# Kernel tuning notes

Hardware: AMD Instinct MI355X
Metric: run time of the kernel (lower is better)

## Reference

```python
import jax, jax.numpy as jnp
import numpy as np

DIM = 2048
DIM_INNER = 4096
D_STATE = 64
D_CONV = 4
HEADDIM = 128
NHEADS = DIM_INNER // HEADDIM  # 32
CHUNK = 256
BATCH = 1
SEQ = 2048
CONV_DIM = DIM_INNER + 2 * D_STATE           # 4224
D_IN_PROJ = 2 * DIM_INNER + 2 * D_STATE + NHEADS  # 8352


def setup_inputs() -> dict:
    key = jax.random.key(0)
    ks = jax.random.split(key, 8)
    x = jax.random.normal(ks[0], (BATCH, SEQ, DIM), jnp.float32)
    in_proj_w = jax.random.normal(ks[1], (D_IN_PROJ, DIM), jnp.float32) * 0.02
    conv_w = jax.random.normal(ks[2], (CONV_DIM, D_CONV), jnp.float32) * 0.2
    conv_b = jnp.zeros((CONV_DIM,), jnp.float32)
    dt_bias = jax.random.normal(ks[3], (NHEADS,), jnp.float32) * 0.1
    A_log = jnp.log(jax.random.uniform(ks[4], (NHEADS,), jnp.float32, 1.0, 16.0))
    D = jnp.ones((NHEADS,), jnp.float32)
    norm_w = jnp.ones((DIM_INNER,), jnp.float32)
    out_proj_w = jax.random.normal(ks[5], (DIM, DIM_INNER), jnp.float32) * 0.02
    return dict(x=x, in_proj_w=in_proj_w, conv_w=conv_w, conv_b=conv_b,
                dt_bias=dt_bias, A_log=A_log, D=D, norm_w=norm_w,
                out_proj_w=out_proj_w)


def _segsum(a):
    # a: [..., T]; out[..., i, j] = sum_{k=j+1..i} a[..., k] for i>=j else -inf
    T = a.shape[-1]
    cs = jnp.cumsum(a, axis=-1)
    seg = cs[..., :, None] - cs[..., None, :]
    mask = jnp.tril(jnp.ones((T, T), bool))
    return jnp.where(mask, seg, -jnp.inf)


def _ssd(x, A, Bm, Cm, chunk):
    # x: [b,l,h,p], A: [b,l,h], Bm/Cm: [b,l,n] (ngroups=1, group dim squeezed)
    b, l, h, p = x.shape
    n = Bm.shape[-1]
    c = l // chunk
    x = x.reshape(b, c, chunk, h, p)
    A = A.reshape(b, c, chunk, h).transpose(0, 3, 1, 2)  # [b,h,c,l]
    Bm = Bm.reshape(b, c, chunk, n)
    Cm = Cm.reshape(b, c, chunk, n)
    A_cumsum = jnp.cumsum(A, axis=-1)                    # [b,h,c,l]
    Lmat = jnp.exp(_segsum(A))                           # [b,h,c,l,l]
    # intra-chunk (diagonal) contribution
    Y_diag = jnp.einsum('bcln,bcsn,bhcls,bcshp->bclhp', Cm, Bm, Lmat, x)
    # per-chunk states
    decay_states = jnp.exp(A_cumsum[..., -1:] - A_cumsum)
    states = jnp.einsum('bcln,bhcl,bclhp->bchpn', Bm, decay_states, x)
    states = jnp.concatenate([jnp.zeros_like(states[:, :1]), states], axis=1)
    # inter-chunk recurrence
    A_last = jnp.pad(A_cumsum[..., -1], ((0, 0), (0, 0), (1, 0)))  # [b,h,c+1]
    decay_chunk = jnp.exp(_segsum(A_last))
    new_states = jnp.einsum('bhzc,bchpn->bzhpn', decay_chunk, states)
    states, final_state = new_states[:, :-1], new_states[:, -1]
    # state -> output (off-diagonal) contribution
    state_decay_out = jnp.exp(A_cumsum)
    Y_off = jnp.einsum('bcln,bchpn,bhcl->bclhp', Cm, states, state_decay_out)
    return (Y_diag + Y_off).reshape(b, l, h, p), final_state


def reference(x, in_proj_w, conv_w, conv_b, dt_bias, A_log, D, norm_w, out_proj_w):
    B, L, _ = x.shape
    zxbcdt = x @ in_proj_w.T                              # [B,L,8352]
    z = zxbcdt[..., :DIM_INNER]
    xBC = zxbcdt[..., DIM_INNER:DIM_INNER + CONV_DIM]
    dt = jax.nn.softplus(zxbcdt[..., -NHEADS:] + dt_bias)  # [B,L,H]
    # causal depthwise conv1d over time (pad d_conv-1 on the left)
    xc = xBC.transpose(0, 2, 1)                           # [B,conv_dim,L]
    xc = jax.lax.conv_general_dilated(
        xc, conv_w[:, None, :], (1,), [(D_CONV - 1, 0)],
        dimension_numbers=('NCH', 'OIH', 'NCH'), feature_group_count=CONV_DIM)
    xc = xc + conv_b[None, :, None]
    xBC = jax.nn.silu(xc).transpose(0, 2, 1)              # [B,L,conv_dim]
    xs = xBC[..., :DIM_INNER].reshape(B, L, NHEADS, HEADDIM)
    Bmat = xBC[..., DIM_INNER:DIM_INNER + D_STATE]
    Cmat = xBC[..., DIM_INNER + D_STATE:]
    A = -jnp.exp(A_log)                                   # [H]
    y, final_state = _ssd(xs * dt[..., None], A * dt, Bmat, Cmat, CHUNK)
    y = y + xs * D[:, None]
    y = y.reshape(B, L, DIM_INNER)
    # gated RMSNorm: x * silu(z), then rms_norm with weight
    g = y * jax.nn.silu(z)
    g = g * jax.lax.rsqrt(jnp.mean(g * g, axis=-1, keepdims=True) + 1e-5) * norm_w
    return g @ out_proj_w.T
```

## Files before the change

kernel.cpp:

```cpp
#include <hip/hip_runtime.h>

typedef short v8s __attribute__((ext_vector_type(8)));
typedef float v4f __attribute__((ext_vector_type(4)));

#define L_SEQ  2048
#define DPROJ  8352
#define CONVD  4224
#define DIN    4096
#define NH     32
#define HD     128
#define NSTATE 64
#define NCHUNK 8
#define CKLEN  256

#define GLOAD_LDS16(gp, lp) \
  __builtin_amdgcn_global_load_lds((const __attribute__((address_space(1))) void*)(gp), \
                                   (__attribute__((address_space(3))) void*)(lp), 16, 0, 0)

__device__ __forceinline__ unsigned short to_bf16(float f) {
  unsigned u = __float_as_uint(f);
  return (unsigned short)((u + 0x7fffu + ((u >> 16) & 1u)) >> 16);
}

__global__ void cvt_bf16_kernel(const float* __restrict__ in,
                                unsigned short* __restrict__ out, int n) {
  int i = (blockIdx.x * 256 + threadIdx.x) * 8;
  if (i + 8 <= n) {
    float4 a = *(const float4*)(in + i);
    float4 b = *(const float4*)(in + i + 4);
    v8s r;
    r[0] = (short)to_bf16(a.x); r[1] = (short)to_bf16(a.y);
    r[2] = (short)to_bf16(a.z); r[3] = (short)to_bf16(a.w);
    r[4] = (short)to_bf16(b.x); r[5] = (short)to_bf16(b.y);
    r[6] = (short)to_bf16(b.z); r[7] = (short)to_bf16(b.w);
    *(v8s*)(out + i) = r;
  }
}

__global__ __launch_bounds__(256) void gemm_nt_bf16(
    const unsigned short* __restrict__ A, const unsigned short* __restrict__ B,
    float* __restrict__ C, int M, int N, int K)
{
  __shared__ unsigned short As[128 * 32];
  __shared__ unsigned short Bs[128 * 32];
  const int m0 = blockIdx.x * 128;
  const int n0 = blockIdx.y * 128;
  const int tid = threadIdx.x;
  const int wave = tid >> 6, lane = tid & 63;
  const int wm = (wave & 1) * 64, wn = (wave >> 1) * 64;
  const int lrow = lane & 15, lquad = lane >> 4;

  v4f acc[4][4] = {};

  for (int k0 = 0; k0 < K; k0 += 32) {
    __syncthreads();
#pragma unroll
    for (int r = 0; r < 2; ++r) {
      int e = wave * 128 + r * 64 + lane;
      int row = e >> 2;
      int kq = (e & 3) * 8;
      const unsigned short* ap = A + (size_t)(m0 + row) * K + k0 + kq;
      GLOAD_LDS16(ap, As + wave * 1024 + r * 512);
      int br = n0 + row; if (br >= N) br = N - 1;
      const unsigned short* bp = B + (size_t)br * K + k0 + kq;
      GLOAD_LDS16(bp, Bs + wave * 1024 + r * 512);
    }
    __syncthreads();
    v8s af[4], bfr[4];
#pragma unroll
    for (int i = 0; i < 4; ++i)
      af[i] = *(const v8s*)&As[(wm + i * 16 + lrow) * 32 + lquad * 8];
#pragma unroll
    for (int j = 0; j < 4; ++j)
      bfr[j] = *(const v8s*)&Bs[(wn + j * 16 + lrow) * 32 + lquad * 8];
#pragma unroll
    for (int i = 0; i < 4; ++i)
#pragma unroll
      for (int j = 0; j < 4; ++j)
        acc[i][j] = __builtin_amdgcn_mfma_f32_16x16x32_bf16(af[i], bfr[j], acc[i][j], 0, 0, 0);
  }

#pragma unroll
  for (int i = 0; i < 4; ++i) {
    int grow = m0 + wm + i * 16 + lquad * 4;
#pragma unroll
    for (int j = 0; j < 4; ++j) {
      int gcol = n0 + wn + j * 16 + lrow;
      if (gcol < N) {
#pragma unroll
        for (int r = 0; r < 4; ++r)
          C[(size_t)(grow + r) * N + gcol] = acc[i][j][r];
      }
    }
  }
}

__global__ __launch_bounds__(256) void gemm_nt_bf16_64(
    const unsigned short* __restrict__ A, const unsigned short* __restrict__ B,
    float* __restrict__ C, int M, int N, int K)
{
  __shared__ unsigned short As[64 * 32];
  __shared__ unsigned short Bs[128 * 32];
  const int m0 = blockIdx.x * 64;
  const int n0 = blockIdx.y * 128;
  const int tid = threadIdx.x;
  const int wave = tid >> 6, lane = tid & 63;
  const int wm = (wave & 1) * 32, wn = (wave >> 1) * 64;
  const int lrow = lane & 15, lquad = lane >> 4;

  v4f acc[2][4] = {};

  for (int k0 = 0; k0 < K; k0 += 32) {
    __syncthreads();
    {
      int e = wave * 64 + lane;
      int row = e >> 2;
      int kq = (e & 3) * 8;
      const unsigned short* ap = A + (size_t)(m0 + row) * K + k0 + kq;
      GLOAD_LDS16(ap, As + wave * 512);
    }
#pragma unroll
    for (int r = 0; r < 2; ++r) {
      int e = wave * 128 + r * 64 + lane;
      int row = e >> 2;
      int kq = (e & 3) * 8;
      const unsigned short* bp = B + (size_t)(n0 + row) * K + k0 + kq;
      GLOAD_LDS16(bp, Bs + wave * 1024 + r * 512);
    }
    __syncthreads();
    v8s af[2], bfr[4];
#pragma unroll
    for (int i = 0; i < 2; ++i)
      af[i] = *(const v8s*)&As[(wm + i * 16 + lrow) * 32 + lquad * 8];
#pragma unroll
    for (int j = 0; j < 4; ++j)
      bfr[j] = *(const v8s*)&Bs[(wn + j * 16 + lrow) * 32 + lquad * 8];
#pragma unroll
    for (int i = 0; i < 2; ++i)
#pragma unroll
      for (int j = 0; j < 4; ++j)
        acc[i][j] = __builtin_amdgcn_mfma_f32_16x16x32_bf16(af[i], bfr[j], acc[i][j], 0, 0, 0);
  }

#pragma unroll
  for (int i = 0; i < 2; ++i) {
    int grow = m0 + wm + i * 16 + lquad * 4;
#pragma unroll
    for (int j = 0; j < 4; ++j) {
      int gcol = n0 + wn + j * 16 + lrow;
#pragma unroll
      for (int r = 0; r < 4; ++r)
        C[(size_t)(grow + r) * N + gcol] = acc[i][j][r];
    }
  }
}

__global__ __launch_bounds__(256) void conv_silu_kernel(
    const float* __restrict__ zx, const float* __restrict__ cw,
    const float* __restrict__ cb, float* __restrict__ out)
{
  const int l0 = blockIdx.x * 32, c0 = blockIdx.y * 128;
  const int tid = threadIdx.x;
  __shared__ float zs[35][128];
  __shared__ float cwl[4][128];
  __shared__ float cbl[128];
  for (int e = tid; e < 35 * 128; e += 256) {
    int k = e >> 7, cc = e & 127;
    int l = l0 + k - 3;
    zs[k][cc] = (l >= 0) ? zx[(size_t)l * DPROJ + DIN + c0 + cc] : 0.f;
  }
  for (int e = tid; e < 512; e += 256)
    cwl[e & 3][e >> 2] = cw[c0 * 4 + e];
  if (tid < 128) cbl[tid] = cb[c0 + tid];
  __syncthreads();
#pragma unroll
  for (int i = 0; i < 16; ++i) {
    int idx = i * 256 + tid;
    int ll = idx >> 7, cc = idx & 127;
    float acc = cbl[cc];
#pragma unroll
    for (int j = 0; j < 4; ++j)
      acc += zs[ll + j][cc] * cwl[j][cc];
    out[(size_t)(l0 + ll) * CONVD + c0 + cc] = acc / (1.f + __expf(-acc));
  }
}

__global__ void dt_kernel(const float* __restrict__ zx,
                          const float* __restrict__ dtb,
                          float* __restrict__ dt)
{
  int e = blockIdx.x * 256 + threadIdx.x;
  int l = e >> 5, h = e & 31;
  float v = zx[(size_t)l * DPROJ + (DPROJ - NH) + h] + dtb[h];
  dt[e] = (v > 20.f) ? v : log1pf(__expf(v));
}

__global__ void acum_kernel(const float* __restrict__ dt,
                            const float* __restrict__ alog,
                            float* __restrict__ acum)
{
  int h = blockIdx.x & 31, c = blockIdx.x >> 5;
  int t = threadIdx.x;
  int l = c * CKLEN + t;
  float A = -__expf(alog[h]);
  __shared__ float s[256];
  s[t] = A * dt[l * NH + h];
  __syncthreads();
  for (int off = 1; off < 256; off <<= 1) {
    float add = (t >= off) ? s[t - off] : 0.f;
    __syncthreads();
    s[t] += add;
    __syncthreads();
  }
  acum[h * L_SEQ + l] = s[t];
}

__global__ __launch_bounds__(256) void prep_kernel(
    const float* __restrict__ xbc, const float* __restrict__ dt,
    const float* __restrict__ acum, unsigned short* __restrict__ Xd,
    unsigned short* __restrict__ Btw, unsigned short* __restrict__ Cbf)
{
  const int h = blockIdx.x & 31, c = blockIdx.x >> 5;
  const int tid = threadIdx.x;
  __shared__ float Ac[256], Dt[256], Wd[256];
  __shared__ float Xs[32][129];
  __shared__ float Bs2[32][65];
  int l = c * CKLEN + tid;
  float a = acum[h * L_SEQ + l];
  Ac[tid] = a;
  Dt[tid] = dt[l * NH + h];
  __syncthreads();
  float alast = Ac[255];
  Wd[tid] = __expf(fminf(alast - a, 0.f));
  __syncthreads();
  unsigned short* XdB = Xd + (size_t)(c * NH + h) * (HD * CKLEN);
  unsigned short* BtB = Btw + (size_t)(c * NH + h) * (NSTATE * CKLEN);
  for (int t0 = 0; t0 < CKLEN; t0 += 32) {
    for (int e = tid; e < 32 * 128; e += 256) {
      int tt = e >> 7, pp = e & 127;
      Xs[tt][pp] = xbc[(size_t)(c * CKLEN + t0 + tt) * CONVD + h * HD + pp];
    }
    for (int e = tid; e < 32 * 64; e += 256) {
      int tt = e >> 6, nn = e & 63;
      Bs2[tt][nn] = xbc[(size_t)(c * CKLEN + t0 + tt) * CONVD + DIN + nn];
    }
    __syncthreads();
    {
      int p = tid >> 1, th = (tid & 1) * 16;
      v8s r0, r1;
#pragma unroll
      for (int k = 0; k < 8; ++k) {
        r0[k] = (short)to_bf16(Xs[th + k][p] * Dt[t0 + th + k]);
        r1[k] = (short)to_bf16(Xs[th + 8 + k][p] * Dt[t0 + th + 8 + k]);
      }
      *(v8s*)&XdB[p * CKLEN + t0 + th] = r0;
      *(v8s*)&XdB[p * CKLEN + t0 + th + 8] = r1;
    }
    {
      int n = tid >> 2, tq = (tid & 3) * 8;
      v8s r;
#pragma unroll
      for (int k = 0; k < 8; ++k)
        r[k] = (short)to_bf16(Bs2[tq + k][n] * Wd[t0 + tq + k]);
      *(v8s*)&BtB[n * CKLEN + t0 + tq] = r;
    }
    __syncthreads();
  }
  if (h == 0) {
    for (int e = tid; e < CKLEN * NSTATE; e += 256) {
      int ll = e >> 6, nn = e & 63;
      Cbf[(size_t)c * (CKLEN * NSTATE) + e] =
          to_bf16(xbc[(size_t)(c * CKLEN + ll) * CONVD + DIN + NSTATE + nn]);
    }
  }
}

__global__ __launch_bounds__(256) void g_kernel(const float* __restrict__ xbc,
                                                float* __restrict__ G)
{
  int c = blockIdx.z;
  int l0 = blockIdx.y * 64, s0 = blockIdx.x * 64;
  __shared__ float Cs[64][65];
  __shared__ float Bs[64][65];
  int tid = threadIdx.x;
  for (int e = tid; e < 64 * 64; e += 256) {
    int r = e >> 6, k = e & 63;
    Cs[r][k] = xbc[(size_t)(c * CKLEN + l0 + r) * CONVD + DIN + NSTATE + k];
    Bs[r][k] = xbc[(size_t)(c * CKLEN + s0 + r) * CONVD + DIN + k];
  }
  __syncthreads();
  int tx = tid & 15, ty = tid >> 4;
  float acc[4][4] = {};
  for (int k = 0; k < 64; ++k) {
    float a[4], b[4];
#pragma unroll
    for (int i = 0; i < 4; ++i) a[i] = Cs[ty * 4 + i][k];
#pragma unroll
    for (int j = 0; j < 4; ++j) b[j] = Bs[tx * 4 + j][k];
#pragma unroll
    for (int i = 0; i < 4; ++i)
#pragma unroll
      for (int j = 0; j < 4; ++j) acc[i][j] += a[i] * b[j];
  }
  for (int i = 0; i < 4; ++i)
    for (int j = 0; j < 4; ++j)
      G[((size_t)c * CKLEN + l0 + ty * 4 + i) * CKLEN + s0 + tx * 4 + j] = acc[i][j];
}

__global__ __launch_bounds__(256) void gexp_kernel_v2(
    const float* __restrict__ G, const float* __restrict__ acum,
    unsigned short* __restrict__ Gexp)
{
  const int b = blockIdx.x;
  const int si = b & 7, li = (b >> 3) & 3, c = b >> 5;
  const int l0 = li * 64, s0 = si * 32;
  const int tid = threadIdx.x;
  const int r = tid >> 2, sc = (tid & 3) * 8;

  if (s0 >= l0 + 64) {
    v8s z = {};
    for (int h = 0; h < NH; ++h)
      *(v8s*)&Gexp[(size_t)(c * NH + h) * 65536 + (size_t)(l0 + r) * 256 + s0 + sc] = z;
    return;
  }

  __shared__ float Gs[64 * 32];
  __shared__ float Acl[32][64];
  __shared__ float Acs[32][32];
  for (int e = tid; e < 2048; e += 256) {
    int rr = e >> 5, cc = e & 31;
    Gs[e] = G[(size_t)c * 65536 + (size_t)(l0 + rr) * 256 + s0 + cc];
  }
  for (int e = tid; e < 2048; e += 256) {
    int hh = e >> 6, rr = e & 63;
    Acl[hh][rr] = acum[hh * L_SEQ + c * CKLEN + l0 + rr];
  }
  for (int e = tid; e < 1024; e += 256) {
    int hh = e >> 5, ss = e & 31;
    Acs[hh][ss] = acum[hh * L_SEQ + c * CKLEN + s0 + ss];
  }
  __syncthreads();

  float g8[8];
#pragma unroll
  for (int k = 0; k < 8; ++k) g8[k] = Gs[r * 32 + sc + k];

  for (int h = 0; h < NH; ++h) {
    float al = Acl[h][r];
    v8s o;
#pragma unroll
    for (int k = 0; k < 8; ++k) {
      int s = s0 + sc + k;
      float m = 0.f;
      if (s <= l0 + r) m = g8[k] * __expf(fminf(al - Acs[h][sc + k], 0.f));
      o[k] = (short)to_bf16(m);
    }
    *(v8s*)&Gexp[(size_t)(c * NH + h) * 65536 + (size_t)(l0 + r) * 256 + s0 + sc] = o;
  }
}

__global__ __launch_bounds__(256) void states_kernel_v2(
    const unsigned short* __restrict__ Xd, const unsigned short* __restrict__ Btw,
    float* __restrict__ st)
{
  const int h = blockIdx.x & 31, c = blockIdx.x >> 5;
  const int tid = threadIdx.x;
  const int wave = tid >> 6, lane = tid & 63;
  const int wm = (wave & 1) * 64, wn = (wave >> 1) * 32;
  const int lrow = lane & 15, lquad = lane >> 4;

  __shared__ unsigned short As[128 * 32];
  __shared__ unsigned short Bs[64 * 32];
  const unsigned short* Ab = Xd + (size_t)(c * NH + h) * (HD * CKLEN);
  const unsigned short* Bb = Btw + (size_t)(c * NH + h) * (NSTATE * CKLEN);

  v4f acc[4][2] = {};

  for (int k0 = 0; k0 < CKLEN; k0 += 32) {
    __syncthreads();
#pragma unroll
    for (int r = 0; r < 2; ++r) {
      int e = wave * 128 + r * 64 + lane;
      int row = e >> 2, kq = (e & 3) * 8;
      GLOAD_LDS16(Ab + (size_t)row * CKLEN + k0 + kq, As + wave * 1024 + r * 512);
    }
    {
      int e = wave * 64 + lane;
      int row = e >> 2, kq = (e & 3) * 8;
      GLOAD_LDS16(Bb + (size_t)row * CKLEN + k0 + kq, Bs + wave * 512);
    }
    __syncthreads();
    v8s af[4], bfr[2];
#pragma unroll
    for (int i = 0; i < 4; ++i)
      af[i] = *(const v8s*)&As[(wm + i * 16 + lrow) * 32 + lquad * 8];
#pragma unroll
    for (int j = 0; j < 2; ++j)
      bfr[j] = *(const v8s*)&Bs[(wn + j * 16 + lrow) * 32 + lquad * 8];
#pragma unroll
    for (int i = 0; i < 4; ++i)
#pragma unroll
      for (int j = 0; j < 2; ++j)
        acc[i][j] = __builtin_amdgcn_mfma_f32_16x16x32_bf16(af[i], bfr[j], acc[i][j], 0, 0, 0);
  }

  float* outp = st + (size_t)(c * NH + h) * (HD * NSTATE);
#pragma unroll
  for (int i = 0; i < 4; ++i) {
    int p0 = wm + i * 16 + lquad * 4;
#pragma unroll
    for (int j = 0; j < 2; ++j) {
      int n = wn + j * 16 + lrow;
#pragma unroll
      for (int r = 0; r < 4; ++r)
        outp[(size_t)(p0 + r) * NSTATE + n] = acc[i][j][r];
    }
  }
}

__global__ void scan_kernel(const float* __restrict__ acum,
                            const float* __restrict__ st,
                            unsigned short* __restrict__ spbf)
{
  int e = blockIdx.x * 256 + threadIdx.x;
  int h = e >> 13;
  float running = 0.f;
#pragma unroll
  for (int c = 0; c < NCHUNK; ++c) {
    spbf[(size_t)c * 262144 + e] = to_bf16(running);
    float dec = __expf(fminf(acum[h * L_SEQ + c * CKLEN + 255], 0.f));
    running = running * dec + st[(size_t)c * 262144 + e];
  }
}

__global__ __launch_bounds__(256) void y_kernel_v2(
    const unsigned short* __restrict__ Gexp, const unsigned short* __restrict__ Xd,
    const unsigned short* __restrict__ Cbf, const unsigned short* __restrict__ spbf,
    const float* __restrict__ xbc, const float* __restrict__ acum,
    const float* __restrict__ Dp, float* __restrict__ Y)
{
  const int b = blockIdx.x, h = blockIdx.y, c = blockIdx.z;
  const int tid = threadIdx.x;
  const int wave = tid >> 6, lane = tid & 63;
  const int wm = wave * 32;
  const int lrow = lane & 15, lquad = lane >> 4;

  __shared__ unsigned short As[128 * 32];
  __shared__ unsigned short Bs[128 * 32];

  v4f acc[2][8] = {};

  const unsigned short* Ca = Cbf + (size_t)c * (CKLEN * NSTATE) + (size_t)b * 128 * NSTATE;
  const unsigned short* Sb = spbf + (size_t)(c * NH + h) * (HD * NSTATE);
  for (int n0 = 0; n0 < NSTATE; n0 += 32) {
    __syncthreads();
#pragma unroll
    for (int r = 0; r < 2; ++r) {
      int e = wave * 128 + r * 64 + lane;
      int row = e >> 2, kq = (e & 3) * 8;
      GLOAD_LDS16(Ca + (size_t)row * NSTATE + n0 + kq, As + wave * 1024 + r * 512);
      GLOAD_LDS16(Sb + (size_t)row * NSTATE + n0 + kq, Bs + wave * 1024 + r * 512);
    }
    __syncthreads();
    v8s af[2], bfr[8];
#pragma unroll
    for (int i = 0; i < 2; ++i)
      af[i] = *(const v8s*)&As[(wm + i * 16 + lrow) * 32 + lquad * 8];
#pragma unroll
    for (int j = 0; j < 8; ++j)
      bfr[j] = *(const v8s*)&Bs[(j * 16 + lrow) * 32 + lquad * 8];
#pragma unroll
    for (int i = 0; i < 2; ++i)
#pragma unroll
      for (int j = 0; j < 8; ++j)
        acc[i][j] = __builtin_amdgcn_mfma_f32_16x16x32_bf16(af[i], bfr[j], acc[i][j], 0, 0, 0);
  }

#pragma unroll
  for (int i = 0; i < 2; ++i) {
#pragma unroll
    for (int r = 0; r < 4; ++r) {
      int Lg = c * CKLEN + b * 128 + wm + i * 16 + lquad * 4 + r;
      float eA = __expf(fminf(acum[h * L_SEQ + Lg], 0.f));
#pragma unroll
      for (int j = 0; j < 8; ++j) acc[i][j][r] *= eA;
    }
  }

  const unsigned short* Ga = Gexp + (size_t)(c * NH + h) * (CKLEN * CKLEN)
                           + (size_t)b * 128 * CKLEN;
  const unsigned short* Xb = Xd + (size_t)(c * NH + h) * (HD * CKLEN);

  const int smax = (b + 1) * 128;
  for (int s0 = 0; s0 < smax; s0 += 32) {
    __syncthreads();
#pragma unroll
    for (int r = 0; r < 2; ++r) {
      int e = wave * 128 + r * 64 + lane;
      int row = e >> 2, kq = (e & 3) * 8;
      GLOAD_LDS16(Ga + (size_t)row * CKLEN + s0 + kq, As + wave * 1024 + r * 512);
      GLOAD_LDS16(Xb + (size_t)row * CKLEN + s0 + kq, Bs + wave * 1024 + r * 512);
    }
    __syncthreads();
    if (s0 <= b * 128 + wm + 31) {
      v8s af[2], bfr[8];
#pragma unroll
      for (int i = 0; i < 2; ++i)
        af[i] = *(const v8s*)&As[(wm + i * 16 + lrow) * 32 + lquad * 8];
#pragma unroll
      for (int j = 0; j < 8; ++j)
        bfr[j] = *(const v8s*)&Bs[(j * 16 + lrow) * 32 + lquad * 8];
#pragma unroll
      for (int i = 0; i < 2; ++i)
#pragma unroll
        for (int j = 0; j < 8; ++j)
          acc[i][j] = __builtin_amdgcn_mfma_f32_16x16x32_bf16(af[i], bfr[j], acc[i][j], 0, 0, 0);
    }
  }

  const float Dh = Dp[h];
#pragma unroll
  for (int i = 0; i < 2; ++i) {
#pragma unroll
    for (int j = 0; j < 8; ++j) {
      int p = j * 16 + lrow;
#pragma unroll
      for (int r = 0; r < 4; ++r) {
        int Lg = c * CKLEN + b * 128 + wm + i * 16 + lquad * 4 + r;
        float xs = xbc[(size_t)Lg * CONVD + h * HD + p];
        Y[(size_t)Lg * DIN + h * HD + p] = acc[i][j][r] + Dh * xs;
      }
    }
  }
}

__global__ __launch_bounds__(256) void norm_gate_kernel(const float* __restrict__ Y,
                                                        const float* __restrict__ zx,
                                                        const float* __restrict__ nw,
                                                        unsigned short* __restrict__ gbf)
{
  int l = blockIdx.x;
  int t = threadIdx.x;
  float g[16];
  float ss = 0.f;
#pragma unroll
  for (int i = 0; i < 16; ++i) {
    int idx = i * 256 + t;
    float z = zx[(size_t)l * DPROJ + idx];
    float y = Y[(size_t)l * DIN + idx];
    float gv = y * (z / (1.f + __expf(-z)));
    g[i] = gv;
    ss += gv * gv;
  }
#pragma unroll
  for (int off = 32; off > 0; off >>= 1) ss += __shfl_down(ss, off);
  __shared__ float red[4];
  if ((t & 63) == 0) red[t >> 6] = ss;
  __syncthreads();
  float total = red[0] + red[1] + red[2] + red[3];
  float scale = rsqrtf(total / (float)DIN + 1e-5f);
#pragma unroll
  for (int i = 0; i < 16; ++i) {
    int idx = i * 256 + t;
    gbf[(size_t)l * DIN + idx] = to_bf16(g[i] * scale * nw[idx]);
  }
}

extern "C" void kernel_launch(void* const* d_in, const int* in_sizes, int n_in,
                              void* d_out, int out_size, void* d_ws, size_t ws_size,
                              hipStream_t stream) {
  const float* x    = (const float*)d_in[0];
  const float* w1   = (const float*)d_in[1];
  const float* cw   = (const float*)d_in[2];
  const float* cb   = (const float*)d_in[3];
  const float* dtb  = (const float*)d_in[4];
  const float* alog = (const float*)d_in[5];
  const float* Dp   = (const float*)d_in[6];
  const float* nw   = (const float*)d_in[7];
  const float* w2   = (const float*)d_in[8];
  float* out = (float*)d_out;
  float* ws  = (float*)d_ws;

  unsigned short* xbf  = (unsigned short*)(ws + 0);
  unsigned short* w1bf = (unsigned short*)(ws + 2097152);
  unsigned short* Gexp = (unsigned short*)(ws + 0);
  unsigned short* Btw  = (unsigned short*)(ws + 8388608);
  unsigned short* w2bf = (unsigned short*)(ws + 10649600);
  float* zx   = ws + 14843904;
  float* xbc  = ws + 31948800;
  float* dt   = ws + 40599552;
  float* acum = ws + 40665088;
  float* G    = ws + 40730624;
  float* st   = ws + 41254912;
  float* Y    = ws + 43352064;
  unsigned short* gbf  = (unsigned short*)(ws + 51740672);
  unsigned short* Xd   = (unsigned short*)(ws + 53837824);
  unsigned short* Cbf  = (unsigned short*)(ws + 58032128);
  unsigned short* spbf = (unsigned short*)(ws + 58097664);

  cvt_bf16_kernel<<<4194304 / 2048, 256, 0, stream>>>(x, xbf, 4194304);
  cvt_bf16_kernel<<<17104896 / 2048, 256, 0, stream>>>(w1, w1bf, 17104896);
  cvt_bf16_kernel<<<8388608 / 2048, 256, 0, stream>>>(w2, w2bf, 8388608);

  gemm_nt_bf16<<<dim3(16, 66), 256, 0, stream>>>(xbf, w1bf, zx, 2048, 8352, 2048);

  conv_silu_kernel<<<dim3(64, 33), 256, 0, stream>>>(zx, cw, cb, xbc);
  dt_kernel<<<(L_SEQ * NH) / 256, 256, 0, stream>>>(zx, dtb, dt);
  acum_kernel<<<NCHUNK * NH, 256, 0, stream>>>(dt, alog, acum);

  prep_kernel<<<NCHUNK * NH, 256, 0, stream>>>(xbc, dt, acum, Xd, Btw, Cbf);
  g_kernel<<<dim3(4, 4, NCHUNK), 256, 0, stream>>>(xbc, G);
  gexp_kernel_v2<<<256, 256, 0, stream>>>(G, acum, Gexp);

  states_kernel_v2<<<NCHUNK * NH, 256, 0, stream>>>(Xd, Btw, st);
  scan_kernel<<<262144 / 256, 256, 0, stream>>>(acum, st, spbf);
  y_kernel_v2<<<dim3(2, NH, NCHUNK), 256, 0, stream>>>(Gexp, Xd, Cbf, spbf, xbc, acum, Dp, Y);

  norm_gate_kernel<<<L_SEQ, 256, 0, stream>>>(Y, zx, nw, gbf);

  gemm_nt_bf16_64<<<dim3(32, 16), 256, 0, stream>>>(gbf, w2bf, out, 2048, 2048, 4096);
}
```

Baseline: 498.8 us.

## Replace in-projection GEMM with 256x256 double-buffered pipelined MFMA kernel

Replaces the 128x128, K=32 single-buffered in_proj GEMM with a 256x256-tile, 512-thread kernel using K=64 tiles. The LDS is double-buffered with XOR swizzling, and global-to-LDS loads are interleaved with MFMA quarter-steps using explicit waitcnt, barriers and setprio. The goal is to raise arithmetic intensity, hide load latency and cut LDS bank conflicts. The cost is 128KB of shared memory per block and fewer blocks (8x33) over the 256 CUs, with padding waste on the last N tile.

```diff
diff --git a/kernel.cpp b/kernel.cpp
--- a/kernel.cpp
+++ b/kernel.cpp
@@ -37,62 +37,146 @@
   }
 }
 
-__global__ __launch_bounds__(256) void gemm_nt_bf16(
+
+#define BAR    __builtin_amdgcn_s_barrier()
+#define SCHEDB __builtin_amdgcn_sched_barrier(0)
+#define LGKM0  asm volatile("s_waitcnt lgkmcnt(0)" ::: "memory")
+#define VMCNT4 asm volatile("s_waitcnt vmcnt(4)" ::: "memory")
+
+#define RDA(bu, mh) do { \
+  _Pragma("unroll") \
+  for (int i = 0; i < 4; ++i) \
+    _Pragma("unroll") \
+    for (int s = 0; s < 2; ++s) { \
+      int row_ = (mh) * 128 + wm * 64 + i * 16 + lrow; \
+      int off_ = row_ * 128 + s * 64 + lquad * 16; \
+      off_ ^= ((off_ >> 9) & 1) << 5; \
+      a8[i][s] = *(const v8s*)((const char*)smem + (bu) * 32768 + off_); \
+    } \
+} while (0)
+
+#define RDB(bu, nh) do { \
+  _Pragma("unroll") \
+  for (int j = 0; j < 2; ++j) \
+    _Pragma("unroll") \
+    for (int s = 0; s < 2; ++s) { \
+      int row_ = (nh) * 128 + wn * 32 + j * 16 + lrow; \
+      int off_ = row_ * 128 + s * 64 + lquad * 16; \
+      off_ ^= ((off_ >> 9) & 1) << 5; \
+      b8[nh][j][s] = *(const v8s*)((const char*)smem + 65536 + (bu) * 32768 + off_); \
+    } \
+} while (0)
+
+#define MM(mh, nh) do { \
+  __builtin_amdgcn_s_setprio(1); \
+  _Pragma("unroll") \
+  for (int i = 0; i < 4; ++i) \
+    _Pragma("unroll") \
+    for (int j = 0; j < 2; ++j) \
+      _Pragma("unroll") \
+      for (int s = 0; s < 2; ++s) \
+        acc[(mh)*4+i][(nh)*2+j] = __builtin_amdgcn_mfma_f32_16x16x32_bf16( \
+            a8[i][s], b8[(nh)][j][s], acc[(mh)*4+i][(nh)*2+j], 0, 0, 0); \
+  __builtin_amdgcn_s_setprio(0); \
+} while (0)
+
+#define KSTEP(BU, BN_, T1, T2) do { \
+  RDA(BU, 0); RDB(BU, 0); \
+  stA(BN_, 1, T1); \
+  BAR; SCHEDB; LGKM0; SCHEDB; \
+  MM(0, 0); \
+  BAR; SCHEDB; \
+  RDB(BU, 1); \
+  stB(BN_, 1, T1); \
+  BAR; SCHEDB; LGKM0; SCHEDB; \
+  MM(0, 1); \
+  BAR; SCHEDB; \
+  RDA(BU, 1); \
+  stA(BU, 0, T2); \
+  BAR; SCHEDB; LGKM0; SCHEDB; \
+  MM(1, 0); \
+  BAR; SCHEDB; \
+  stB(BU, 0, T2); \
+  BAR; SCHEDB; \
+  MM(1, 1); \
+  VMCNT4; SCHEDB; \
+  BAR; SCHEDB; \
+} while (0)
+
+__global__ __launch_bounds__(512, 2) void gemm_nt_256(
     const unsigned short* __restrict__ A, const unsigned short* __restrict__ B,
     float* __restrict__ C, int M, int N, int K)
 {
-  __shared__ unsigned short As[128 * 32];
-  __shared__ unsigned short Bs[128 * 32];
-  const int m0 = blockIdx.x * 128;
-  const int n0 = blockIdx.y * 128;
+  __shared__ unsigned short smem[65536];
+  const int m0 = blockIdx.x * 256;
+  const int n0 = blockIdx.y * 256;
   const int tid = threadIdx.x;
   const int wave = tid >> 6, lane = tid & 63;
-  const int wm = (wave & 1) * 64, wn = (wave >> 1) * 64;
+  const int wm = wave >> 2, wn = wave & 3;
   const int lrow = lane & 15, lquad = lane >> 4;
-
-  v4f acc[4][4] = {};
-
-  for (int k0 = 0; k0 < K; k0 += 32) {
-    __syncthreads();
-#pragma unroll
-    for (int r = 0; r < 2; ++r) {
-      int e = wave * 128 + r * 64 + lane;
-      int row = e >> 2;
-      int kq = (e & 3) * 8;
-      const unsigned short* ap = A + (size_t)(m0 + row) * K + k0 + kq;
-      GLOAD_LDS16(ap, As + wave * 1024 + r * 512);
-      int br = n0 + row; if (br >= N) br = N - 1;
-      const unsigned short* bp = B + (size_t)br * K + k0 + kq;
-      GLOAD_LDS16(bp, Bs + wave * 1024 + r * 512);
-    }
-    __syncthreads();
-    v8s af[4], bfr[4];
-#pragma unroll
-    for (int i = 0; i < 4; ++i)
-      af[i] = *(const v8s*)&As[(wm + i * 16 + lrow) * 32 + lquad * 8];
-#pragma unroll
-    for (int j = 0; j < 4; ++j)
-      bfr[j] = *(const v8s*)&Bs[(wn + j * 16 + lrow) * 32 + lquad * 8];
-#pragma unroll
-    for (int i = 0; i < 4; ++i)
-#pragma unroll
-      for (int j = 0; j < 4; ++j)
-        acc[i][j] = __builtin_amdgcn_mfma_f32_16x16x32_bf16(af[i], bfr[j], acc[i][j], 0, 0, 0);
-  }
-
-#pragma unroll
-  for (int i = 0; i < 4; ++i) {
-    int grow = m0 + wm + i * 16 + lquad * 4;
-#pragma unroll
-    for (int j = 0; j < 4; ++j) {
-      int gcol = n0 + wn + j * 16 + lrow;
-      if (gcol < N) {
-#pragma unroll
-        for (int r = 0; r < 4; ++r)
-          C[(size_t)(grow + r) * N + gcol] = acc[i][j][r];
-      }
-    }
-  }
+  const int NT = K >> 6;
+
+  v4f acc[8][4] = {};
+  v8s a8[4][2];
+  v8s b8[2][2][2];
+
+  auto stA = [&](int bu, int h, int kt) {
+#pragma unroll
+    for (int g = 0; g < 2; ++g) {
+      int lin = h * 16384 + g * 8192 + tid * 16;
+      int sw = lin ^ (((lin >> 9) & 1) << 5);
+      int row = sw >> 7;
+      const unsigned short* src = A + (size_t)(m0 + row) * K + kt * 64 + ((sw & 127) >> 1);
+      GLOAD_LDS16(src, smem + bu * 16384 + h * 8192 + g * 4096 + wave * 512);
+    }
+  };
+  auto stB = [&](int bu, int h, int kt) {
+#pragma unroll
+    for (int g = 0; g < 2; ++g) {
+      int lin = h * 16384 + g * 8192 + tid * 16;
+      int sw = lin ^ (((lin >> 9) & 1) << 5);
+      int brow = n0 + (sw >> 7);
+      if (brow >= N) brow = N - 1;
+      const unsigned short* src = B + (size_t)brow * K + kt * 64 + ((sw & 127) >> 1);
+      GLOAD_LDS16(src, smem + 32768 + bu * 16384 + h * 8192 + g * 4096 + wave * 512);
+    }
+  };
+
+  stA(0, 0, 0); stA(0, 1, 0); stB(0, 0, 0); stB(0, 1, 0);
+  stA(1, 0, 1); stB(1, 0, 1);
+  VMCNT4; SCHEDB; BAR; SCHEDB;
+
+#pragma unroll 1
+  for (int tt = 0; tt < NT; tt += 2) {
+    {
+      int t1 = tt + 1;
+      int t2 = (tt + 2 < NT) ? tt + 2 : NT - 1;
+      KSTEP(0, 1, t1, t2);
+    }
+    {
+      int t1 = (tt + 2 < NT) ? tt + 2 : NT - 1;
+      int t2 = (tt + 3 < NT) ? tt + 3 : NT - 1;
+      KSTEP(1, 0, t1, t2);
+    }
+  }
+
+#pragma unroll
+  for (int mh = 0; mh < 2; ++mh)
+#pragma unroll
+    for (int i = 0; i < 4; ++i) {
+      int grow = m0 + mh * 128 + wm * 64 + i * 16 + lquad * 4;
+#pragma unroll
+      for (int nh = 0; nh < 2; ++nh)
+#pragma unroll
+        for (int j = 0; j < 2; ++j) {
+          int gcol = n0 + nh * 128 + wn * 32 + j * 16 + lrow;
+          if (gcol < N) {
+#pragma unroll
+            for (int r = 0; r < 4; ++r)
+              C[(size_t)(grow + r) * N + gcol] = acc[mh * 4 + i][nh * 2 + j][r];
+          }
+        }
+    }
 }
 
 __global__ __launch_bounds__(256) void gemm_nt_bf16_64(
@@ -602,7 +686,7 @@
   cvt_bf16_kernel<<<17104896 / 2048, 256, 0, stream>>>(w1, w1bf, 17104896);
   cvt_bf16_kernel<<<8388608 / 2048, 256, 0, stream>>>(w2, w2bf, 8388608);
 
-  gemm_nt_bf16<<<dim3(16, 66), 256, 0, stream>>>(xbf, w1bf, zx, 2048, 8352, 2048);
+  gemm_nt_256<<<dim3(8, 33), 512, 0, stream>>>(xbf, w1bf, zx, 2048, 8352, 2048);
 
   conv_silu_kernel<<<dim3(64, 33), 256, 0, stream>>>(zx, cw, cb, xbc);
   dt_kernel<<<(L_SEQ * NH) / 256, 256, 0, stream>>>(zx, dtb, dt);
```

New measurement: 498.4 us. No clear change (-0.1%).
